# Kernel optimization log

Measured on AMD Instinct MI355X. Metric: run time of the kernel, lower is better.

Reference implementation:

```python
import jax, jax.numpy as jnp
import numpy as np

B, S, D = 1, 2048, 1024
H, DK = 16, 64
DFF, E, K = 4096, 8, 2
EPS = float(np.finfo(np.float32).eps)  # torch nn.RMSNorm default eps = finfo.eps


def setup_inputs() -> dict:
    key = jax.random.key(0)
    ks = jax.random.split(key, 8)
    s = 0.02
    return {
        "x": jax.random.normal(ks[0], (B, S, D), jnp.float32),
        "qkv_w": jax.random.normal(ks[1], (3 * D, D), jnp.float32) * s,
        "out_w": jax.random.normal(ks[2], (D, D), jnp.float32) * s,
        "router_w": jax.random.normal(ks[3], (E, D), jnp.float32) * s,
        "w1": jax.random.normal(ks[4], (E, DFF, D), jnp.float32) * s,
        "w2": jax.random.normal(ks[5], (E, D, DFF), jnp.float32) * s,
        "norm1_w": jnp.ones((D,), jnp.float32),
        "norm2_w": jnp.ones((D,), jnp.float32),
    }


def _rmsnorm(x, w):
    return x * jax.lax.rsqrt(jnp.mean(x * x, axis=-1, keepdims=True) + EPS) * w


def _rope(x):
    # x: [B, S, H, dk]; rotate-half RoPE as in RotaryPositionalEmbedding
    dk = x.shape[-1]
    inv_freq = 1.0 / (10000.0 ** (jnp.arange(0, dk, 2, dtype=jnp.float32) / dk))
    t = jnp.arange(x.shape[1], dtype=jnp.float32)
    freqs = t[:, None] * inv_freq[None, :]          # [S, dk/2]
    cos = jnp.cos(freqs)[None, :, None, :]
    sin = jnp.sin(freqs)[None, :, None, :]
    x1, x2 = jnp.split(x, 2, axis=-1)
    return jnp.concatenate([x1 * cos - x2 * sin, x2 * cos + x1 * sin], axis=-1)


def _block(x, qkv_w, out_w, router_w, w1, w2, norm1_w, norm2_w):
    Bv, Sv, Dv = x.shape
    # --- attention with RoPE (causal, eval mode) ---
    h = _rmsnorm(x, norm1_w)
    qkv = (h @ qkv_w.T).reshape(Bv, Sv, 3, H, DK)
    q, k, v = qkv[:, :, 0], qkv[:, :, 1], qkv[:, :, 2]   # [B,S,H,dk]
    q = _rope(q)
    k = _rope(k)
    scores = jnp.einsum('bshd,bthd->bhst', q, k) / np.float32(np.sqrt(DK))
    causal = jnp.tril(jnp.ones((Sv, Sv), dtype=bool))
    scores = jnp.where(causal, scores, jnp.float32(-jnp.inf))
    attn = jax.nn.softmax(scores, axis=-1)
    o = jnp.einsum('bhst,bthd->bshd', attn, v).reshape(Bv, Sv, Dv)
    x = x + o @ out_w.T
    # --- MoE with top-k routing ---
    h2 = _rmsnorm(x, norm2_w).reshape(-1, Dv)            # [T, D]
    logits = h2 @ router_w.T                             # [T, E]
    probs = jax.nn.softmax(logits, axis=-1)
    top_p, top_i = jax.lax.top_k(probs, K)               # [T, K]
    top_p = top_p / jnp.sum(top_p, axis=-1, keepdims=True)
    T = h2.shape[0]
    # dense per-token per-expert combine weights (same math as masked loop)
    w_dense = jnp.zeros((T, E), h2.dtype).at[jnp.arange(T)[:, None], top_i].add(top_p)
    hid = jax.nn.gelu(jnp.einsum('td,efd->etf', h2, w1), approximate=False)  # [E,T,DFF]
    eo = jnp.einsum('etf,edf->etd', hid, w2)                                  # [E,T,D]
    moe = jnp.einsum('etd,te->td', eo, w_dense).reshape(Bv, Sv, Dv)
    aux_loss = E * jnp.sum(jnp.mean(probs, axis=0) ** 2)
    return x + moe, aux_loss


def reference(x, qkv_w, out_w, router_w, w1, w2, norm1_w, norm2_w):
    return _block(x, qkv_w, out_w, router_w, w1, w2, norm1_w, norm2_w)
```

## Files before the change

### kernel.cpp

```cpp
#include <hip/hip_runtime.h>
#include <cstdint>
#include <math.h>

typedef float f32x4 __attribute__((ext_vector_type(4)));
typedef __bf16 bf16x8 __attribute__((ext_vector_type(8)));
typedef unsigned short us4 __attribute__((ext_vector_type(4)));

#define DEV static __device__ __forceinline__

DEV unsigned short f2bf(float f){
  union { __bf16 h; unsigned short u; } cv; cv.h = (__bf16)f; return cv.u;
}
DEV float bf2f(unsigned short u){ return __uint_as_float((unsigned int)u << 16); }

DEV void gload16(const void* g, void* l){
  __builtin_amdgcn_global_load_lds((__attribute__((address_space(1))) void*)g,
                                   (__attribute__((address_space(3))) void*)l, 16, 0, 0);
}

__global__ __launch_bounds__(256) void rmsnorm_kernel(const float* __restrict__ x, const float* __restrict__ w,
    unsigned short* __restrict__ ob){
  int t = blockIdx.x, tid = threadIdx.x;
  float4 xv = *(const float4*)(x + (long long)t*1024 + tid*4);
  float ss = xv.x*xv.x + xv.y*xv.y + xv.z*xv.z + xv.w*xv.w;
  for (int m=32;m;m>>=1) ss += __shfl_xor(ss,m);
  __shared__ float lds[4];
  if ((tid&63)==0) lds[tid>>6] = ss;
  __syncthreads();
  float tot = lds[0]+lds[1]+lds[2]+lds[3];
  float inv = rsqrtf(tot*(1.0f/1024.0f) + 1.1920928955078125e-07f);
  float4 wv = *(const float4*)(w + tid*4);
  us4 rb = { f2bf(xv.x*inv*wv.x), f2bf(xv.y*inv*wv.y), f2bf(xv.z*inv*wv.z), f2bf(xv.w*inv*wv.w) };
  *(us4*)&ob[(long long)t*1024 + tid*4] = rb;
}

__global__ __launch_bounds__(256) void rmsnorm2_kernel(const float* __restrict__ xp, int ksn, long long kstride,
    const float* __restrict__ w, float* __restrict__ x1, unsigned short* __restrict__ hb, float* __restrict__ hf){
  int t = blockIdx.x, tid = threadIdx.x;
  long long b = (long long)t*1024 + tid*4;
  float4 xv = {0.f,0.f,0.f,0.f};
  for (int ks=0; ks<ksn; ++ks){
    float4 a = *(const float4*)(xp + ks*kstride + b);
    xv.x+=a.x; xv.y+=a.y; xv.z+=a.z; xv.w+=a.w;
  }
  *(float4*)(x1 + b) = xv;
  float ss = xv.x*xv.x + xv.y*xv.y + xv.z*xv.z + xv.w*xv.w;
  for (int m=32;m;m>>=1) ss += __shfl_xor(ss,m);
  __shared__ float lds[4];
  if ((tid&63)==0) lds[tid>>6] = ss;
  __syncthreads();
  float tot = lds[0]+lds[1]+lds[2]+lds[3];
  float inv = rsqrtf(tot*(1.0f/1024.0f) + 1.1920928955078125e-07f);
  float4 wv = *(const float4*)(w + tid*4);
  float r0 = xv.x*inv*wv.x, r1 = xv.y*inv*wv.y, r2 = xv.z*inv*wv.z, r3 = xv.w*inv*wv.w;
  us4 rb = { f2bf(r0), f2bf(r1), f2bf(r2), f2bf(r3) };
  *(us4*)&hb[b] = rb;
  float4 rf; rf.x=r0; rf.y=r1; rf.z=r2; rf.w=r3;
  *(float4*)(hf + b) = rf;
}

template<int EPI, bool GATHER>
__global__ __launch_bounds__(256) void gemm_bt(
    const unsigned short* __restrict__ A, int lda,
    const float* __restrict__ Bw, long long bstride, int ldb,
    int M, int N, int K, int KS, long long ksoff,
    const int* __restrict__ counts, const int* __restrict__ offs,
    const int* __restrict__ tok_list, const float* __restrict__ wgt,
    const float* __restrict__ resid,
    float* __restrict__ Cf, unsigned short* __restrict__ Cb, int ldc)
{
  const int z = blockIdx.z;
  const int e = z / KS, ks = z - e*KS;
  const int Me = counts ? counts[e] : M;
  const int by = blockIdx.y;
  if (by * 128 >= Me) return;
  const int rbase = offs ? offs[e] : 0;
  const int bx = blockIdx.x;
  const float* B = Bw + (long long)e * bstride;
  const int kn = K / KS;
  const int kbeg = ks * kn;
  const int nt = kn >> 5;

  __shared__ __align__(16) char smem[3*24576];

  const int tid = threadIdx.x, lane = tid & 63, w = tid >> 6;
  const int wr = w >> 1, wc = w & 1;

  const unsigned short* asrc[2];
  #pragma unroll
  for (int i = 0; i < 2; ++i){
    int G = tid + i*256;
    int R = G >> 2, c = G & 3;
    int cg = c ^ ((R>>1)&3);
    int lr = by*128 + R; if (lr >= Me) lr = Me-1;
    int li = rbase + lr;
    int ar = GATHER ? (tok_list[li] >> 1) : li;
    asrc[i] = A + (long long)ar * lda + kbeg + cg*8;
  }
  const float* bsrc[4];
  #pragma unroll
  for (int i = 0; i < 4; ++i){
    int G = tid + i*256;
    int R = G >> 3, c = G & 7;
    int cg = c ^ (R & 7);
    bsrc[i] = B + (long long)(bx*128 + R) * ldb + kbeg + cg*4;
  }

  f32x4 acc[4][4] = {};

  auto stage = [&](int b, int kof){
    char* s = smem + b*24576;
    #pragma unroll
    for (int i = 0; i < 2; ++i) gload16(asrc[i] + kof, s + (i*256 + w*64)*16);
    #pragma unroll
    for (int i = 0; i < 4; ++i) gload16(bsrc[i] + kof, s + 8192 + (i*256 + w*64)*16);
  };

  stage(0, 0);
  if (nt > 1) stage(1, 32);
  if (nt > 2) stage(2, 64);

  int buf = 0;
  for (int t = 0; t < nt; ++t){
    if (t + 2 < nt)      { asm volatile("s_waitcnt vmcnt(12)" ::: "memory"); }
    else if (t + 1 < nt) { asm volatile("s_waitcnt vmcnt(6)"  ::: "memory"); }
    else                 { asm volatile("s_waitcnt vmcnt(0)"  ::: "memory"); }
    __builtin_amdgcn_sched_barrier(0);
    __builtin_amdgcn_s_barrier();
    __builtin_amdgcn_sched_barrier(0);

    const char* abase = smem + buf*24576;
    const char* bbase = abase + 8192;
    bf16x8 af[4], bfr[4];
    #pragma unroll
    for (int m=0;m<4;++m){
      int R = wr*64 + m*16 + (lane&15);
      int c = (lane>>4) ^ ((R>>1)&3);
      af[m] = *(const bf16x8*)(abase + R*64 + c*16);
    }
    #pragma unroll
    for (int n=0;n<4;++n){
      int R = wc*64 + n*16 + (lane&15);
      int c0 = ((lane>>4)*2) ^ (R&7);
      int c1 = c0 ^ 1;
      f32x4 v0 = *(const f32x4*)(bbase + R*128 + c0*16);
      f32x4 v1 = *(const f32x4*)(bbase + R*128 + c1*16);
      bf16x8 tt;
      tt[0]=(__bf16)v0[0]; tt[1]=(__bf16)v0[1]; tt[2]=(__bf16)v0[2]; tt[3]=(__bf16)v0[3];
      tt[4]=(__bf16)v1[0]; tt[5]=(__bf16)v1[1]; tt[6]=(__bf16)v1[2]; tt[7]=(__bf16)v1[3];
      bfr[n] = tt;
    }
    #pragma unroll
    for (int m=0;m<4;++m)
      #pragma unroll
      for (int n=0;n<4;++n)
        acc[m][n] = __builtin_amdgcn_mfma_f32_16x16x32_bf16(af[m], bfr[n], acc[m][n], 0, 0, 0);

    __builtin_amdgcn_sched_barrier(0);
    __builtin_amdgcn_s_barrier();
    __builtin_amdgcn_sched_barrier(0);
    if (t + 3 < nt) stage(buf, (t+3)*32);
    buf = (buf == 2) ? 0 : buf + 1;
  }

  #pragma unroll
  for (int m=0;m<4;++m){
    #pragma unroll
    for (int r=0;r<4;++r){
      int lr = by*128 + wr*64 + m*16 + 4*(lane>>4) + r;
      if (lr >= Me) continue;
      #pragma unroll
      for (int n=0;n<4;++n){
        int col = bx*128 + wc*64 + n*16 + (lane&15);
        float v = acc[m][n][r];
        if constexpr (EPI == 1){
          if (ks == 0) v += resid[(long long)lr*ldc + col];
          Cf[ks*ksoff + (long long)lr*ldc + col] = v;
        } else if constexpr (EPI == 2){
          float g = 0.5f * v * (1.0f + erff(v * 0.70710678118654752f));
          Cb[(long long)(rbase+lr)*ldc + col] = f2bf(g);
        } else if constexpr (EPI == 3){
          int gi = rbase + lr;
          int ts = tok_list[gi];
          Cf[ks*ksoff + (long long)ts*ldc + col] = v * wgt[gi];
        } else {
          Cb[(long long)lr*ldc + col] = f2bf(v);
        }
      }
    }
  }
}

__global__ __launch_bounds__(256) void rope_kernel(const unsigned short* __restrict__ qkvb,
    unsigned short* __restrict__ q, unsigned short* __restrict__ k){
  int t = blockIdx.x, tid = threadIdx.x;
  const unsigned short* row = qkvb + (long long)t*3072;
  #pragma unroll
  for (int u2=0; u2<2; ++u2){
    int pid = tid + u2*256;
    int hh = pid >> 5, j = pid & 31;
    float invf = __expf(-(float)j * 0.28782313662425575f);
    float fr = (float)t * invf;
    float sn, cs;
    __sincosf(fr, &sn, &cs);
    int base = hh*64 + j;
    long long ob_ = (long long)t*1024 + base;
    float a = bf2f(row[base]), b = bf2f(row[base+32]);
    q[ob_]    = f2bf(a*cs - b*sn);
    q[ob_+32] = f2bf(b*cs + a*sn);
    a = bf2f(row[1024+base]); b = bf2f(row[1024+base+32]);
    k[ob_]    = f2bf(a*cs - b*sn);
    k[ob_+32] = f2bf(b*cs + a*sn);
  }
}

__global__ __launch_bounds__(256) void attn_kernel(
    const unsigned short* __restrict__ Q,
    const unsigned short* __restrict__ K,
    const unsigned short* __restrict__ V, int ldv,
    unsigned short* __restrict__ O)
{
  const int bx = blockIdx.x, h = blockIdx.y;
  const int q0 = bx*64;
  const int tid = threadIdx.x, lane = tid&63, w = tid>>6;

  __shared__ __align__(16) unsigned short Ks[64*64];
  __shared__ __align__(16) unsigned short Vs[64*64];
  __shared__ __align__(16) unsigned short Ps[4*16*64];
  unsigned short* Pw = Ps + w*1024;

  const int qrow = q0 + w*16 + (lane&15);
  bf16x8 aq[2];
  #pragma unroll
  for (int kk=0;kk<2;++kk)
    aq[kk] = *(const bf16x8*)&Q[(long long)qrow*1024 + h*64 + 32*kk + 8*(lane>>4)];

  f32x4 o[4] = {};
  float Mx[4] = {-INFINITY,-INFINITY,-INFINITY,-INFINITY};
  float Ls[4] = {0.f,0.f,0.f,0.f};

  const int row_g = q0 + w*16 + 4*(lane>>4);
  const int nt = bx + 1;
  for (int it = 0; it < nt; ++it){
    int k0 = it*64;
    #pragma unroll
    for (int i=0;i<2;++i){
      int seg = 4*i + w;
      int row = seg*8 + (lane>>3);
      int cs = (lane&7) ^ (row&7);
      gload16(&K[(long long)(k0+row)*1024 + h*64 + cs*8], &Ks[seg*512]);
      gload16(&V[(long long)(k0+row)*ldv  + h*64 + cs*8], &Vs[seg*512]);
    }
    __syncthreads();
    f32x4 st[4];
    #pragma unroll
    for (int kt=0;kt<4;++kt){
      f32x4 s = {0.f,0.f,0.f,0.f};
      #pragma unroll
      for (int kk=0;kk<2;++kk){
        int R = kt*16 + (lane&15);
        int ch = ((lane>>4)+4*kk) ^ (R&7);
        bf16x8 bk = *(const bf16x8*)&Ks[R*64 + ch*8];
        s = __builtin_amdgcn_mfma_f32_16x16x32_bf16(aq[kk], bk, s, 0,0,0);
      }
      st[kt] = s;
    }
    #pragma unroll
    for (int kt=0;kt<4;++kt){
      int col = k0 + kt*16 + (lane&15);
      #pragma unroll
      for (int r=0;r<4;++r){
        float vv = st[kt][r]*0.125f;
        st[kt][r] = (col <= row_g + r) ? vv : -INFINITY;
      }
    }
    float sf[4];
    #pragma unroll
    for (int r=0;r<4;++r){
      float mx = fmaxf(fmaxf(st[0][r],st[1][r]),fmaxf(st[2][r],st[3][r]));
      mx = fmaxf(mx, __shfl_xor(mx,1));
      mx = fmaxf(mx, __shfl_xor(mx,2));
      mx = fmaxf(mx, __shfl_xor(mx,4));
      mx = fmaxf(mx, __shfl_xor(mx,8));
      float mn = fmaxf(Mx[r], mx);
      float sc = __expf(Mx[r]-mn);
      Mx[r]=mn; sf[r]=sc;
      float ls=0.f;
      #pragma unroll
      for (int kt=0;kt<4;++kt){ float pp = __expf(st[kt][r]-mn); st[kt][r]=pp; ls+=pp; }
      Ls[r] = Ls[r]*sc + ls;
    }
    #pragma unroll
    for (int dt=0;dt<4;++dt)
      #pragma unroll
      for (int r=0;r<4;++r) o[dt][r] *= sf[r];
    #pragma unroll
    for (int kt=0;kt<4;++kt)
      #pragma unroll
      for (int r=0;r<4;++r){
        int prow = 4*(lane>>4)+r, pcol = kt*16+(lane&15);
        int byteoff = (prow*128 + pcol*2) ^ ((prow&7)<<4);
        *(unsigned short*)((char*)Pw + byteoff) = f2bf(st[kt][r]);
      }
    bf16x8 pa[2];
    #pragma unroll
    for (int kk=0;kk<2;++kk){
      int pr = lane&15;
      int ch = ((lane>>4)+4*kk) ^ (pr&7);
      pa[kk] = *(const bf16x8*)&Pw[pr*64 + ch*8];
    }
    #pragma unroll
    for (int dt=0;dt<4;++dt){
      #pragma unroll
      for (int kk=0;kk<2;++kk){
        union { unsigned short u[8]; bf16x8 v; } Ub;
        #pragma unroll
        for (int j=0;j<8;++j){
          int kr = 32*kk + 8*(lane>>4) + j;
          int d = dt*16 + (lane&15);
          int byteoff = (kr*128 + d*2) ^ ((kr&7)<<4);
          Ub.u[j] = *(const unsigned short*)((const char*)Vs + byteoff);
        }
        o[dt] = __builtin_amdgcn_mfma_f32_16x16x32_bf16(pa[kk], Ub.v, o[dt], 0,0,0);
      }
    }
    __syncthreads();
  }
  #pragma unroll
  for (int r=0;r<4;++r){
    float l = Ls[r];
    l += __shfl_xor(l,1); l += __shfl_xor(l,2); l += __shfl_xor(l,4); l += __shfl_xor(l,8);
    Ls[r] = 1.0f / l;
  }
  #pragma unroll
  for (int dt=0;dt<4;++dt)
    #pragma unroll
    for (int r=0;r<4;++r){
      float vv = o[dt][r]*Ls[r];
      int rg = row_g + r;
      O[(long long)rg*1024 + h*64 + dt*16 + (lane&15)] = f2bf(vv);
    }
}

__global__ __launch_bounds__(256) void router_kernel(const float* __restrict__ h2f, const float* __restrict__ rw,
    float* __restrict__ probs, int* __restrict__ tope, float* __restrict__ topw, int* __restrict__ counts){
  int t = blockIdx.x, tid = threadIdx.x;
  float4 hv = *(const float4*)(h2f + (long long)t*1024 + tid*4);
  float pe[8];
  #pragma unroll
  for (int e2=0;e2<8;++e2){
    float4 wv = *(const float4*)(rw + e2*1024 + tid*4);
    pe[e2] = hv.x*wv.x + hv.y*wv.y + hv.z*wv.z + hv.w*wv.w;
  }
  __shared__ float lds[32];
  #pragma unroll
  for (int e2=0;e2<8;++e2){
    float v = pe[e2];
    for (int m=32;m;m>>=1) v += __shfl_xor(v,m);
    if ((tid&63)==0) lds[(tid>>6)*8+e2] = v;
  }
  __syncthreads();
  if (tid==0){
    float lg[8], pp[8];
    #pragma unroll
    for (int e2=0;e2<8;++e2) lg[e2] = lds[e2]+lds[8+e2]+lds[16+e2]+lds[24+e2];
    float mx = lg[0];
    for (int e2=1;e2<8;++e2) mx = fmaxf(mx, lg[e2]);
    float s = 0.f;
    for (int e2=0;e2<8;++e2){ pp[e2] = __expf(lg[e2]-mx); s += pp[e2]; }
    float inv = 1.0f/s;
    int i0 = 0;
    for (int e2=1;e2<8;++e2) if (pp[e2] > pp[i0]) i0 = e2;
    int i1 = (i0==0)?1:0;
    for (int e2=0;e2<8;++e2) if (e2!=i0 && pp[e2] > pp[i1]) i1 = e2;
    for (int e2=0;e2<8;++e2) probs[t*8+e2] = pp[e2]*inv;
    float p0 = pp[i0], p1 = pp[i1], wsum = p0+p1;
    tope[t*2] = i0; tope[t*2+1] = i1;
    topw[t*2] = p0/wsum; topw[t*2+1] = p1/wsum;
    atomicAdd(&counts[i0],1); atomicAdd(&counts[i1],1);
  }
}

__global__ void init_kernel(int* counts, int* cursor){
  int i = threadIdx.x;
  if (i<8){ counts[i]=0; cursor[i]=0; }
}

__global__ void prefix_kernel(const int* counts, int* offs){
  if (threadIdx.x==0){
    int a=0;
    for (int e2=0;e2<8;++e2){ offs[e2]=a; a+=counts[e2]; }
  }
}

__global__ void scatter_kernel(const int* __restrict__ tope, const float* __restrict__ topw,
    const int* __restrict__ offs, int* __restrict__ cursor, int* __restrict__ tok_list, float* __restrict__ wgt){
  int t = blockIdx.x*blockDim.x + threadIdx.x;
  if (t >= 2048) return;
  #pragma unroll
  for (int s=0;s<2;++s){
    int e2 = tope[t*2+s];
    int pos = atomicAdd(&cursor[e2], 1);
    int i = offs[e2] + pos;
    tok_list[i] = t*2+s;
    wgt[i] = topw[t*2+s];
  }
}

__global__ __launch_bounds__(256) void aux_kernel(const float* __restrict__ probs, float* __restrict__ out){
  int tid = threadIdx.x;
  float pe[8] = {0,0,0,0,0,0,0,0};
  for (int t = tid; t < 2048; t += 256){
    #pragma unroll
    for (int e2=0;e2<8;++e2) pe[e2] += probs[t*8+e2];
  }
  __shared__ float lds[32];
  #pragma unroll
  for (int e2=0;e2<8;++e2){
    float v = pe[e2];
    for (int m=32;m;m>>=1) v += __shfl_xor(v,m);
    if ((tid&63)==0) lds[(tid>>6)*8 + e2] = v;
  }
  __syncthreads();
  if (tid==0){
    float aux = 0.f;
    #pragma unroll
    for (int e2=0;e2<8;++e2){
      float mean = (lds[e2]+lds[8+e2]+lds[16+e2]+lds[24+e2]) * (1.0f/2048.0f);
      aux += mean*mean;
    }
    out[2097152] = 8.0f * aux;
  }
}

__global__ __launch_bounds__(256) void final_kernel(const float* __restrict__ x1, const float* __restrict__ slots,
    int ksn, long long kstride, float* __restrict__ out){
  int t = blockIdx.x, tid = threadIdx.x;
  long long b = (long long)t*1024 + tid*4;
  float4 a = *(const float4*)(x1 + b);
  long long s = (long long)t*2048 + tid*4;
  for (int ks=0; ks<ksn; ++ks){
    float4 s0 = *(const float4*)(slots + ks*kstride + s);
    float4 s1 = *(const float4*)(slots + ks*kstride + s + 1024);
    a.x += s0.x + s1.x; a.y += s0.y + s1.y; a.z += s0.z + s1.z; a.w += s0.w + s1.w;
  }
  *(float4*)(out + b) = a;
}

extern "C" void kernel_launch(void* const* d_in, const int* in_sizes, int n_in,
                              void* d_out, int out_size, void* d_ws, size_t ws_size,
                              hipStream_t stream)
{
  (void)in_sizes; (void)n_in; (void)out_size;
  const float* x    = (const float*)d_in[0];
  const float* qkvw = (const float*)d_in[1];
  const float* outw = (const float*)d_in[2];
  const float* rw   = (const float*)d_in[3];
  const float* w1   = (const float*)d_in[4];
  const float* w2   = (const float*)d_in[5];
  const float* n1w  = (const float*)d_in[6];
  const float* n2w  = (const float*)d_in[7];
  float* out = (float*)d_out;

  char* base = (char*)d_ws;
  const size_t MB = 1ull<<20;
  const bool big = ws_size >= 150*MB;
  const int KSO = big ? 4 : 2;
  const int KSW = 2;

  unsigned short* h_b  = (unsigned short*)(base + 0*MB);
  unsigned short* qb   = (unsigned short*)(base + 4*MB);
  unsigned short* kb   = (unsigned short*)(base + 8*MB);
  unsigned short* ob   = (unsigned short*)(base + 12*MB);
  unsigned short* qkvb = (unsigned short*)(base + 16*MB);
  unsigned short* hid  = (unsigned short*)(base + 0*MB);

  float *x1p, *h2f, *slots, *x1;
  unsigned short* h2b;
  char* small_;
  if (big){
    x1p   = (float*)(base + 32*MB);
    h2f   = (float*)(base + 64*MB);
    slots = (float*)(base + 72*MB);
    x1    = (float*)(base + 136*MB);
    h2b   = (unsigned short*)(base + 144*MB);
    small_ = base + 148*MB;
  } else {
    x1p   = (float*)(base + 32*MB);
    h2f   = (float*)(base + 48*MB);
    slots = (float*)(base + 32*MB);
    x1    = (float*)(base + 64*MB);
    h2b   = (unsigned short*)(base + 72*MB);
    small_ = base + 76*MB;
  }
  float* probs = (float*)(small_);
  int*   tope  = (int*)(small_ + 256*1024);
  float* topw  = (float*)(small_ + 512*1024);
  int*   tok_list = (int*)(small_ + 768*1024);
  float* wgt   = (float*)(small_ + 1024*1024);
  int*   counts= (int*)(small_ + 1536*1024);
  int*   offs  = (int*)(small_ + 1536*1024 + 256);
  int*   cursor= (int*)(small_ + 1536*1024 + 512);

  init_kernel<<<1,64,0,stream>>>(counts, cursor);
  rmsnorm_kernel<<<2048,256,0,stream>>>(x, n1w, h_b);
  gemm_bt<4,false><<<dim3(24,16,1),256,0,stream>>>(h_b,1024, qkvw,0,1024, 2048,3072,1024, 1,0,
      nullptr,nullptr,nullptr,nullptr,nullptr, nullptr,qkvb,3072);
  rope_kernel<<<2048,256,0,stream>>>(qkvb, qb, kb);
  attn_kernel<<<dim3(32,16),256,0,stream>>>(qb, kb, qkvb+2048, 3072, ob);
  gemm_bt<1,false><<<dim3(8,16,KSO),256,0,stream>>>(ob,1024, outw,0,1024, 2048,1024,1024, KSO,(long long)2048*1024,
      nullptr,nullptr,nullptr,nullptr, x, x1p,nullptr,1024);
  rmsnorm2_kernel<<<2048,256,0,stream>>>(x1p, KSO, (long long)2048*1024, n2w, x1, h2b, h2f);
  router_kernel<<<2048,256,0,stream>>>(h2f, rw, probs, tope, topw, counts);
  prefix_kernel<<<1,64,0,stream>>>(counts, offs);
  scatter_kernel<<<8,256,0,stream>>>(tope, topw, offs, cursor, tok_list, wgt);
  gemm_bt<2,true><<<dim3(32,16,8),256,0,stream>>>(h2b,1024, w1,(long long)4096*1024,1024, 2048,4096,1024, 1,0,
      counts,offs,tok_list,nullptr,nullptr, nullptr,hid,4096);
  gemm_bt<3,false><<<dim3(8,16,8*KSW),256,0,stream>>>(hid,4096, w2,(long long)4096*1024,4096, 2048,1024,4096, KSW,(long long)4096*1024,
      counts,offs,tok_list,wgt,nullptr, slots,nullptr,1024);
  aux_kernel<<<1,256,0,stream>>>(probs, out);
  final_kernel<<<2048,256,0,stream>>>(x1, slots, KSW, (long long)4096*1024, out);
}
```

Measured before the change: 457.4 us.

## Enlarge GEMM tiles to 256x256 with 512 threads, XCD-aware remap, double buffering

The bf16 MFMA GEMM moves from 128x128 tiles with 256 threads and triple-buffered LDS to 256x256 tiles with 8 waves and a double-buffered 96KB LDS stage. A flat block-index remap groups consecutive tiles onto the same XCD. The W2 split-K factor rises to 4 when the workspace is large. Bigger tiles raise arithmetic intensity and reuse of the fp32 weights, but they cut the number of blocks a lot (e.g. 96 for QKV, 128 for out-proj), which risks underfilling the CUs and leaves less latency hiding with only two buffers.

New measurement: 515.9 us. +12.8%, slower.

```diff
diff --git a/kernel.cpp b/kernel.cpp
--- a/kernel.cpp
+++ b/kernel.cpp
@@ -60,7 +60,7 @@
 }
 
 template<int EPI, bool GATHER>
-__global__ __launch_bounds__(256) void gemm_bt(
+__global__ __launch_bounds__(512, 2) void gemm_bt(
     const unsigned short* __restrict__ A, int lda,
     const float* __restrict__ Bw, long long bstride, int ldb,
     int M, int N, int K, int KS, long long ksoff,
@@ -69,30 +69,38 @@
     const float* __restrict__ resid,
     float* __restrict__ Cf, unsigned short* __restrict__ Cb, int ldc)
 {
-  const int z = blockIdx.z;
+  const int gx = gridDim.x, gy = gridDim.y, gz = gridDim.z;
+  int flat = blockIdx.x + gx*(blockIdx.y + gy*blockIdx.z);
+  int nwg = gx*gy*gz;
+  int q = nwg >> 3, r = nwg & 7;
+  int xcd = flat & 7, p = flat >> 3;
+  int nf = (xcd < r ? xcd*(q+1) : r*(q+1) + (xcd-r)*q) + p;
+  const int by = nf % gx;
+  int rest = nf / gx;
+  const int bx = rest % gy;
+  const int z  = rest / gy;
+
   const int e = z / KS, ks = z - e*KS;
   const int Me = counts ? counts[e] : M;
-  const int by = blockIdx.y;
-  if (by * 128 >= Me) return;
+  if (by * 256 >= Me) return;
   const int rbase = offs ? offs[e] : 0;
-  const int bx = blockIdx.x;
   const float* B = Bw + (long long)e * bstride;
   const int kn = K / KS;
   const int kbeg = ks * kn;
   const int nt = kn >> 5;
 
-  __shared__ __align__(16) char smem[3*24576];
+  __shared__ __align__(16) char smem[2*49152];
 
   const int tid = threadIdx.x, lane = tid & 63, w = tid >> 6;
-  const int wr = w >> 1, wc = w & 1;
+  const int wr = w >> 2, wc = w & 3;
 
   const unsigned short* asrc[2];
   #pragma unroll
   for (int i = 0; i < 2; ++i){
-    int G = tid + i*256;
+    int G = tid + i*512;
     int R = G >> 2, c = G & 3;
     int cg = c ^ ((R>>1)&3);
-    int lr = by*128 + R; if (lr >= Me) lr = Me-1;
+    int lr = by*256 + R; if (lr >= Me) lr = Me-1;
     int li = rbase + lr;
     int ar = GATHER ? (tok_list[li] >> 1) : li;
     asrc[i] = A + (long long)ar * lda + kbeg + cg*8;
@@ -100,48 +108,46 @@
   const float* bsrc[4];
   #pragma unroll
   for (int i = 0; i < 4; ++i){
-    int G = tid + i*256;
+    int G = tid + i*512;
     int R = G >> 3, c = G & 7;
     int cg = c ^ (R & 7);
-    bsrc[i] = B + (long long)(bx*128 + R) * ldb + kbeg + cg*4;
-  }
-
-  f32x4 acc[4][4] = {};
+    bsrc[i] = B + (long long)(bx*256 + R) * ldb + kbeg + cg*4;
+  }
+
+  f32x4 acc[8][4] = {};
 
   auto stage = [&](int b, int kof){
-    char* s = smem + b*24576;
-    #pragma unroll
-    for (int i = 0; i < 2; ++i) gload16(asrc[i] + kof, s + (i*256 + w*64)*16);
-    #pragma unroll
-    for (int i = 0; i < 4; ++i) gload16(bsrc[i] + kof, s + 8192 + (i*256 + w*64)*16);
+    char* s = smem + b*49152;
+    #pragma unroll
+    for (int i = 0; i < 2; ++i) gload16(asrc[i] + kof, s + (i*512 + tid)*16 - lane*16 + lane*16);
+    #pragma unroll
+    for (int i = 0; i < 4; ++i) gload16(bsrc[i] + kof, s + 16384 + (i*512 + tid)*16 - lane*16 + lane*16);
   };
 
   stage(0, 0);
   if (nt > 1) stage(1, 32);
-  if (nt > 2) stage(2, 64);
-
-  int buf = 0;
+
   for (int t = 0; t < nt; ++t){
-    if (t + 2 < nt)      { asm volatile("s_waitcnt vmcnt(12)" ::: "memory"); }
-    else if (t + 1 < nt) { asm volatile("s_waitcnt vmcnt(6)"  ::: "memory"); }
-    else                 { asm volatile("s_waitcnt vmcnt(0)"  ::: "memory"); }
+    int buf = t & 1;
+    if (t + 1 < nt) { asm volatile("s_waitcnt vmcnt(6)" ::: "memory"); }
+    else            { asm volatile("s_waitcnt vmcnt(0)" ::: "memory"); }
     __builtin_amdgcn_sched_barrier(0);
     __builtin_amdgcn_s_barrier();
     __builtin_amdgcn_sched_barrier(0);
 
-    const char* abase = smem + buf*24576;
-    const char* bbase = abase + 8192;
-    bf16x8 af[4], bfr[4];
-    #pragma unroll
-    for (int m=0;m<4;++m){
-      int R = wr*64 + m*16 + (lane&15);
+    const char* abase = smem + buf*49152;
+    const char* bbase = abase + 16384;
+    bf16x8 af[8], bfr[4];
+    #pragma unroll
+    for (int m=0;m<8;++m){
+      int R = wr*128 + m*16 + (lane&15);
       int c = (lane>>4) ^ ((R>>1)&3);
       af[m] = *(const bf16x8*)(abase + R*64 + c*16);
     }
     #pragma unroll
     for (int n=0;n<4;++n){
       int R = wc*64 + n*16 + (lane&15);
-      int c0 = ((lane>>4)*2) ^ (R&7);
+      int c0 = (2*(lane>>4)) ^ (R&7);
       int c1 = c0 ^ 1;
       f32x4 v0 = *(const f32x4*)(bbase + R*128 + c0*16);
       f32x4 v1 = *(const f32x4*)(bbase + R*128 + c1*16);
@@ -151,7 +157,7 @@
       bfr[n] = tt;
     }
     #pragma unroll
-    for (int m=0;m<4;++m)
+    for (int m=0;m<8;++m)
       #pragma unroll
       for (int n=0;n<4;++n)
         acc[m][n] = __builtin_amdgcn_mfma_f32_16x16x32_bf16(af[m], bfr[n], acc[m][n], 0, 0, 0);
@@ -159,20 +165,19 @@
     __builtin_amdgcn_sched_barrier(0);
     __builtin_amdgcn_s_barrier();
     __builtin_amdgcn_sched_barrier(0);
-    if (t + 3 < nt) stage(buf, (t+3)*32);
-    buf = (buf == 2) ? 0 : buf + 1;
-  }
-
-  #pragma unroll
-  for (int m=0;m<4;++m){
-    #pragma unroll
-    for (int r=0;r<4;++r){
-      int lr = by*128 + wr*64 + m*16 + 4*(lane>>4) + r;
+    if (t + 2 < nt) stage(buf, (t+2)*32);
+  }
+
+  #pragma unroll
+  for (int m=0;m<8;++m){
+    #pragma unroll
+    for (int r2=0;r2<4;++r2){
+      int lr = by*256 + wr*128 + m*16 + 4*(lane>>4) + r2;
       if (lr >= Me) continue;
       #pragma unroll
       for (int n=0;n<4;++n){
-        int col = bx*128 + wc*64 + n*16 + (lane&15);
-        float v = acc[m][n][r];
+        int col = bx*256 + wc*64 + n*16 + (lane&15);
+        float v = acc[m][n][r2];
         if constexpr (EPI == 1){
           if (ks == 0) v += resid[(long long)lr*ldc + col];
           Cf[ks*ksoff + (long long)lr*ldc + col] = v;
@@ -466,7 +471,7 @@
   const size_t MB = 1ull<<20;
   const bool big = ws_size >= 150*MB;
   const int KSO = big ? 4 : 2;
-  const int KSW = 2;
+  const int KSW = big ? 4 : 2;
 
   unsigned short* h_b  = (unsigned short*)(base + 0*MB);
   unsigned short* qb   = (unsigned short*)(base + 4*MB);
@@ -504,19 +509,19 @@
 
   init_kernel<<<1,64,0,stream>>>(counts, cursor);
   rmsnorm_kernel<<<2048,256,0,stream>>>(x, n1w, h_b);
-  gemm_bt<4,false><<<dim3(24,16,1),256,0,stream>>>(h_b,1024, qkvw,0,1024, 2048,3072,1024, 1,0,
+  gemm_bt<4,false><<<dim3(8,12,1),512,0,stream>>>(h_b,1024, qkvw,0,1024, 2048,3072,1024, 1,0,
       nullptr,nullptr,nullptr,nullptr,nullptr, nullptr,qkvb,3072);
   rope_kernel<<<2048,256,0,stream>>>(qkvb, qb, kb);
   attn_kernel<<<dim3(32,16),256,0,stream>>>(qb, kb, qkvb+2048, 3072, ob);
-  gemm_bt<1,false><<<dim3(8,16,KSO),256,0,stream>>>(ob,1024, outw,0,1024, 2048,1024,1024, KSO,(long long)2048*1024,
+  gemm_bt<1,false><<<dim3(8,4,KSO),512,0,stream>>>(ob,1024, outw,0,1024, 2048,1024,1024, KSO,(long long)2048*1024,
       nullptr,nullptr,nullptr,nullptr, x, x1p,nullptr,1024);
   rmsnorm2_kernel<<<2048,256,0,stream>>>(x1p, KSO, (long long)2048*1024, n2w, x1, h2b, h2f);
   router_kernel<<<2048,256,0,stream>>>(h2f, rw, probs, tope, topw, counts);
   prefix_kernel<<<1,64,0,stream>>>(counts, offs);
   scatter_kernel<<<8,256,0,stream>>>(tope, topw, offs, cursor, tok_list, wgt);
-  gemm_bt<2,true><<<dim3(32,16,8),256,0,stream>>>(h2b,1024, w1,(long long)4096*1024,1024, 2048,4096,1024, 1,0,
+  gemm_bt<2,true><<<dim3(8,16,8),512,0,stream>>>(h2b,1024, w1,(long long)4096*1024,1024, 2048,4096,1024, 1,0,
       counts,offs,tok_list,nullptr,nullptr, nullptr,hid,4096);
-  gemm_bt<3,false><<<dim3(8,16,8*KSW),256,0,stream>>>(hid,4096, w2,(long long)4096*1024,4096, 2048,1024,4096, KSW,(long long)4096*1024,
+  gemm_bt<3,false><<<dim3(8,4,8*KSW),512,0,stream>>>(hid,4096, w2,(long long)4096*1024,4096, 2048,1024,4096, KSW,(long long)4096*1024,
       counts,offs,tok_list,wgt,nullptr, slots,nullptr,1024);
   aux_kernel<<<1,256,0,stream>>>(probs, out);
   final_kernel<<<2048,256,0,stream>>>(x1, slots, KSW, (long long)4096*1024, out);
```

## Convert GEMM weights to bf16 in registers before LDS and remap blocks per XCD

Applied to the files above, without the earlier changes.

The GEMM no longer stages fp32 weight tiles into LDS with async loads and converts them to bf16 in every wave. It now loads the weights into registers, converts them once, and writes swizzled bf16 tiles into a double-buffered LDS region. Activations keep a three-stage async-load ring. This cuts LDS use and repeated conversion work, and adds a launch_bounds occupancy hint of 3. Block indices are also remapped so that neighbouring tiles land on the same XCD, the grid dimensions are swapped, and the w2 split-K factor rises to 4 when the workspace is large. The register-staged B path adds register pressure and tighter manual waitcnt ordering.

Measured after the change: 507.6 us. 1.11x slower.

```diff
diff --git a/kernel.cpp b/kernel.cpp
--- a/kernel.cpp
+++ b/kernel.cpp
@@ -5,6 +5,7 @@
 typedef float f32x4 __attribute__((ext_vector_type(4)));
 typedef __bf16 bf16x8 __attribute__((ext_vector_type(8)));
 typedef unsigned short us4 __attribute__((ext_vector_type(4)));
+typedef unsigned short us8 __attribute__((ext_vector_type(8)));
 
 #define DEV static __device__ __forceinline__
 
@@ -60,7 +61,7 @@
 }
 
 template<int EPI, bool GATHER>
-__global__ __launch_bounds__(256) void gemm_bt(
+__global__ __launch_bounds__(256, 3) void gemm_bt(
     const unsigned short* __restrict__ A, int lda,
     const float* __restrict__ Bw, long long bstride, int ldb,
     int M, int N, int K, int KS, long long ksoff,
@@ -69,110 +70,145 @@
     const float* __restrict__ resid,
     float* __restrict__ Cf, unsigned short* __restrict__ Cb, int ldc)
 {
-  const int z = blockIdx.z;
+  const int gx = gridDim.x, gy = gridDim.y;
+  int flat = blockIdx.x + gx*(blockIdx.y + gy*blockIdx.z);
+  int nwg = gx*gy*gridDim.z;
+  int q = nwg >> 3, r = nwg & 7;
+  int xcd = flat & 7, p = flat >> 3;
+  int nf = (xcd < r ? xcd*(q+1) : r*(q+1) + (xcd-r)*q) + p;
+  const int by = nf % gx;
+  int rest = nf / gx;
+  const int bx = rest % gy;
+  const int z  = rest / gy;
+
   const int e = z / KS, ks = z - e*KS;
   const int Me = counts ? counts[e] : M;
-  const int by = blockIdx.y;
   if (by * 128 >= Me) return;
   const int rbase = offs ? offs[e] : 0;
-  const int bx = blockIdx.x;
   const float* B = Bw + (long long)e * bstride;
   const int kn = K / KS;
   const int kbeg = ks * kn;
   const int nt = kn >> 5;
 
-  __shared__ __align__(16) char smem[3*24576];
+  __shared__ __align__(16) char smem[5*8192];
+  char* bufA = smem;
+  char* bufB = smem + 3*8192;
 
   const int tid = threadIdx.x, lane = tid & 63, w = tid >> 6;
   const int wr = w >> 1, wc = w & 1;
 
   const unsigned short* asrc[2];
   #pragma unroll
-  for (int i = 0; i < 2; ++i){
-    int G = tid + i*256;
-    int R = G >> 2, c = G & 3;
+  for (int i=0;i<2;++i){
+    int G = tid + i*256, R = G>>2, c = G&3;
     int cg = c ^ ((R>>1)&3);
     int lr = by*128 + R; if (lr >= Me) lr = Me-1;
     int li = rbase + lr;
     int ar = GATHER ? (tok_list[li] >> 1) : li;
-    asrc[i] = A + (long long)ar * lda + kbeg + cg*8;
-  }
-  const float* bsrc[4];
-  #pragma unroll
-  for (int i = 0; i < 4; ++i){
-    int G = tid + i*256;
-    int R = G >> 3, c = G & 7;
-    int cg = c ^ (R & 7);
-    bsrc[i] = B + (long long)(bx*128 + R) * ldb + kbeg + cg*4;
-  }
+    asrc[i] = A + (long long)ar*lda + kbeg + cg*8;
+  }
+  const int brow0 = tid>>2, bc = tid&3, brow1 = brow0 + 64;
+  const float* bsrc0 = B + (long long)(bx*128 + brow0)*ldb + kbeg + bc*8;
+  const float* bsrc1 = B + (long long)(bx*128 + brow1)*ldb + kbeg + bc*8;
+  const int bws0 = brow0*64 + (bc ^ ((brow0>>1)&3))*16;
+  const int bws1 = brow1*64 + (bc ^ ((brow1>>1)&3))*16;
 
   f32x4 acc[4][4] = {};
 
-  auto stage = [&](int b, int kof){
-    char* s = smem + b*24576;
-    #pragma unroll
-    for (int i = 0; i < 2; ++i) gload16(asrc[i] + kof, s + (i*256 + w*64)*16);
-    #pragma unroll
-    for (int i = 0; i < 4; ++i) gload16(bsrc[i] + kof, s + 8192 + (i*256 + w*64)*16);
+  auto issueA = [&](int t){
+    char* d = bufA + (t%3)*8192;
+    gload16(asrc[0] + t*32, d + tid*16);
+    gload16(asrc[1] + t*32, d + 4096 + tid*16);
   };
-
-  stage(0, 0);
-  if (nt > 1) stage(1, 32);
-  if (nt > 2) stage(2, 64);
-
-  int buf = 0;
-  for (int t = 0; t < nt; ++t){
-    if (t + 2 < nt)      { asm volatile("s_waitcnt vmcnt(12)" ::: "memory"); }
-    else if (t + 1 < nt) { asm volatile("s_waitcnt vmcnt(6)"  ::: "memory"); }
-    else                 { asm volatile("s_waitcnt vmcnt(0)"  ::: "memory"); }
+  auto loadB = [&](int t, f32x4* rb){
+    const f32x4* p0 = (const f32x4*)(bsrc0 + t*32);
+    const f32x4* p1 = (const f32x4*)(bsrc1 + t*32);
+    rb[0] = p0[0]; rb[1] = p0[1];
+    rb[2] = p1[0]; rb[3] = p1[1];
+  };
+  auto writeB = [&](int t, f32x4* rb){
+    char* d = bufB + (t&1)*8192;
+    union { unsigned short u[8]; us8 v; } U0, U1;
+    #pragma unroll
+    for (int j=0;j<4;++j){
+      U0.u[j] = f2bf(rb[0][j]); U0.u[4+j] = f2bf(rb[1][j]);
+      U1.u[j] = f2bf(rb[2][j]); U1.u[4+j] = f2bf(rb[3][j]);
+    }
+    *(us8*)(d + bws0) = U0.v;
+    *(us8*)(d + bws1) = U1.v;
+  };
+  auto compute = [&](int t){
+    const char* ab = bufA + (t%3)*8192;
+    const char* bb = bufB + (t&1)*8192;
+    bf16x8 af[4], bfr[4];
+    #pragma unroll
+    for (int m=0;m<4;++m){
+      int R = wr*64 + m*16 + (lane&15);
+      int c = (lane>>4) ^ ((R>>1)&3);
+      af[m] = *(const bf16x8*)(ab + R*64 + c*16);
+    }
+    #pragma unroll
+    for (int n=0;n<4;++n){
+      int R = wc*64 + n*16 + (lane&15);
+      int c = (lane>>4) ^ ((R>>1)&3);
+      bfr[n] = *(const bf16x8*)(bb + R*64 + c*16);
+    }
+    #pragma unroll
+    for (int m=0;m<4;++m)
+      #pragma unroll
+      for (int n=0;n<4;++n)
+        acc[m][n] = __builtin_amdgcn_mfma_f32_16x16x32_bf16(af[m], bfr[n], acc[m][n], 0, 0, 0);
+  };
+
+  f32x4 rb0[4], rb1[4];
+  issueA(0); loadB(0, rb0);
+  issueA(1); loadB(1, rb1);
+  __builtin_amdgcn_sched_barrier(0);
+  asm volatile("s_waitcnt vmcnt(6)" ::: "memory");
+  __builtin_amdgcn_sched_barrier(0);
+  writeB(0, rb0);
+  asm volatile("s_waitcnt lgkmcnt(0)" ::: "memory");
+  __builtin_amdgcn_sched_barrier(0);
+  __builtin_amdgcn_s_barrier();
+  __builtin_amdgcn_sched_barrier(0);
+
+  for (int t = 0; t < nt; t += 2){
+    if (t+2 < nt){ issueA(t+2); loadB(t+2, rb0); }
+    compute(t);
+    __builtin_amdgcn_sched_barrier(0);
+    if (t+2 < nt){ asm volatile("s_waitcnt vmcnt(6)" ::: "memory"); }
+    else         { asm volatile("s_waitcnt vmcnt(0)" ::: "memory"); }
+    __builtin_amdgcn_sched_barrier(0);
+    writeB(t+1, rb1);
+    asm volatile("s_waitcnt lgkmcnt(0)" ::: "memory");
     __builtin_amdgcn_sched_barrier(0);
     __builtin_amdgcn_s_barrier();
     __builtin_amdgcn_sched_barrier(0);
-
-    const char* abase = smem + buf*24576;
-    const char* bbase = abase + 8192;
-    bf16x8 af[4], bfr[4];
-    #pragma unroll
-    for (int m=0;m<4;++m){
-      int R = wr*64 + m*16 + (lane&15);
-      int c = (lane>>4) ^ ((R>>1)&3);
-      af[m] = *(const bf16x8*)(abase + R*64 + c*16);
-    }
-    #pragma unroll
-    for (int n=0;n<4;++n){
-      int R = wc*64 + n*16 + (lane&15);
-      int c0 = ((lane>>4)*2) ^ (R&7);
-      int c1 = c0 ^ 1;
-      f32x4 v0 = *(const f32x4*)(bbase + R*128 + c0*16);
-      f32x4 v1 = *(const f32x4*)(bbase + R*128 + c1*16);
-      bf16x8 tt;
-      tt[0]=(__bf16)v0[0]; tt[1]=(__bf16)v0[1]; tt[2]=(__bf16)v0[2]; tt[3]=(__bf16)v0[3];
-      tt[4]=(__bf16)v1[0]; tt[5]=(__bf16)v1[1]; tt[6]=(__bf16)v1[2]; tt[7]=(__bf16)v1[3];
-      bfr[n] = tt;
-    }
-    #pragma unroll
-    for (int m=0;m<4;++m)
-      #pragma unroll
-      for (int n=0;n<4;++n)
-        acc[m][n] = __builtin_amdgcn_mfma_f32_16x16x32_bf16(af[m], bfr[n], acc[m][n], 0, 0, 0);
-
+    if (t+3 < nt){ issueA(t+3); loadB(t+3, rb1); }
+    compute(t+1);
+    if (t+2 < nt){
+      __builtin_amdgcn_sched_barrier(0);
+      if (t+3 < nt){ asm volatile("s_waitcnt vmcnt(6)" ::: "memory"); }
+      else         { asm volatile("s_waitcnt vmcnt(0)" ::: "memory"); }
+      __builtin_amdgcn_sched_barrier(0);
+      writeB(t+2, rb0);
+    }
+    asm volatile("s_waitcnt lgkmcnt(0)" ::: "memory");
     __builtin_amdgcn_sched_barrier(0);
     __builtin_amdgcn_s_barrier();
     __builtin_amdgcn_sched_barrier(0);
-    if (t + 3 < nt) stage(buf, (t+3)*32);
-    buf = (buf == 2) ? 0 : buf + 1;
   }
 
   #pragma unroll
   for (int m=0;m<4;++m){
     #pragma unroll
-    for (int r=0;r<4;++r){
-      int lr = by*128 + wr*64 + m*16 + 4*(lane>>4) + r;
+    for (int r2=0;r2<4;++r2){
+      int lr = by*128 + wr*64 + m*16 + 4*(lane>>4) + r2;
       if (lr >= Me) continue;
       #pragma unroll
       for (int n=0;n<4;++n){
         int col = bx*128 + wc*64 + n*16 + (lane&15);
-        float v = acc[m][n][r];
+        float v = acc[m][n][r2];
         if constexpr (EPI == 1){
           if (ks == 0) v += resid[(long long)lr*ldc + col];
           Cf[ks*ksoff + (long long)lr*ldc + col] = v;
@@ -466,7 +502,7 @@
   const size_t MB = 1ull<<20;
   const bool big = ws_size >= 150*MB;
   const int KSO = big ? 4 : 2;
-  const int KSW = 2;
+  const int KSW = big ? 4 : 2;
 
   unsigned short* h_b  = (unsigned short*)(base + 0*MB);
   unsigned short* qb   = (unsigned short*)(base + 4*MB);
@@ -504,19 +540,19 @@
 
   init_kernel<<<1,64,0,stream>>>(counts, cursor);
   rmsnorm_kernel<<<2048,256,0,stream>>>(x, n1w, h_b);
-  gemm_bt<4,false><<<dim3(24,16,1),256,0,stream>>>(h_b,1024, qkvw,0,1024, 2048,3072,1024, 1,0,
+  gemm_bt<4,false><<<dim3(16,24,1),256,0,stream>>>(h_b,1024, qkvw,0,1024, 2048,3072,1024, 1,0,
       nullptr,nullptr,nullptr,nullptr,nullptr, nullptr,qkvb,3072);
   rope_kernel<<<2048,256,0,stream>>>(qkvb, qb, kb);
   attn_kernel<<<dim3(32,16),256,0,stream>>>(qb, kb, qkvb+2048, 3072, ob);
-  gemm_bt<1,false><<<dim3(8,16,KSO),256,0,stream>>>(ob,1024, outw,0,1024, 2048,1024,1024, KSO,(long long)2048*1024,
+  gemm_bt<1,false><<<dim3(16,8,KSO),256,0,stream>>>(ob,1024, outw,0,1024, 2048,1024,1024, KSO,(long long)2048*1024,
       nullptr,nullptr,nullptr,nullptr, x, x1p,nullptr,1024);
   rmsnorm2_kernel<<<2048,256,0,stream>>>(x1p, KSO, (long long)2048*1024, n2w, x1, h2b, h2f);
   router_kernel<<<2048,256,0,stream>>>(h2f, rw, probs, tope, topw, counts);
   prefix_kernel<<<1,64,0,stream>>>(counts, offs);
   scatter_kernel<<<8,256,0,stream>>>(tope, topw, offs, cursor, tok_list, wgt);
-  gemm_bt<2,true><<<dim3(32,16,8),256,0,stream>>>(h2b,1024, w1,(long long)4096*1024,1024, 2048,4096,1024, 1,0,
+  gemm_bt<2,true><<<dim3(16,32,8),256,0,stream>>>(h2b,1024, w1,(long long)4096*1024,1024, 2048,4096,1024, 1,0,
       counts,offs,tok_list,nullptr,nullptr, nullptr,hid,4096);
-  gemm_bt<3,false><<<dim3(8,16,8*KSW),256,0,stream>>>(hid,4096, w2,(long long)4096*1024,4096, 2048,1024,4096, KSW,(long long)4096*1024,
+  gemm_bt<3,false><<<dim3(16,8,8*KSW),256,0,stream>>>(hid,4096, w2,(long long)4096*1024,4096, 2048,1024,4096, KSW,(long long)4096*1024,
       counts,offs,tok_list,wgt,nullptr, slots,nullptr,1024);
   aux_kernel<<<1,256,0,stream>>>(probs, out);
   final_kernel<<<2048,256,0,stream>>>(x1, slots, KSW, (long long)4096*1024, out);
```
